# Kernel tuning notes

Hardware: AMD Instinct MI355X
Metric: run time of the kernel (lower is better)

## Reference

```python
import jax, jax.numpy as jnp
import numpy as np

MAX_IT = 10
LAMBDA_ROF = 4.0
SIGMA = 1.0 / (7.0 * 0.01)
TAU = 0.01
THETA = 0.5
M, N = 2048, 2048


def forward_grad(x):
    """x: [1,M,N] -> [2,M,N]; forward differences, zero at last col/row."""
    gh = jnp.pad(x[0, :, 1:] - x[0, :, :-1], ((0, 0), (0, 1)))  # horizontal
    gv = jnp.pad(x[0, 1:, :] - x[0, :-1, :], ((0, 1), (0, 0)))  # vertical
    return jnp.stack([gh, gv], axis=0)


def backward_div(y):
    """y: [2,M,N] -> [1,M,N]; adjoint backward-difference divergence."""
    yh, yv = y[0], y[1]
    d_h = jnp.concatenate([yh[:, :1], yh[:, 1:-1] - yh[:, :-2], -yh[:, -2:-1]], axis=1)
    d_v = jnp.concatenate([yv[:1, :], yv[1:-1, :] - yv[:-2, :], -yv[-2:-1, :]], axis=0)
    return (d_h + d_v)[None]  # [1,M,N]


def prox_linf_ball(p, r):
    # Torch original builds m1/m2 from p.data (no grad flow) -> stop_gradient.
    m1 = jnp.maximum(p - r, 0.0)
    m2 = jnp.maximum(-p - r, 0.0)
    return p - jax.lax.stop_gradient(m1 - m2)  # == clamp(p, -r, r) in value


def setup_inputs() -> dict:
    key = jax.random.key(0)
    k1, k2 = jax.random.split(key)
    img_obs = jax.random.uniform(k1, (1, M, N), dtype=jnp.float32)
    w1 = jnp.array([0.5], dtype=jnp.float32)  # nn.Parameter [1]
    w2 = jnp.array([0.4], dtype=jnp.float32)  # nn.Parameter [1]
    return {"img_obs": img_obs, "w1": w1, "w2": w2}


def reference(img_obs, w1, w2):
    x = img_obs
    x_tilde = img_obs
    y = forward_grad(x)  # [2,M,N]
    # w_term built from y.data in torch -> constant wrt autodiff
    w_term = jax.lax.stop_gradient(jnp.exp(-jnp.abs(y)))
    w = w1[0] + w2[0] * w_term  # [2,M,N]
    for _ in range(MAX_IT):
        # dual weighted update + L-inf prox
        y = y + SIGMA * w * forward_grad(x_tilde)
        y = prox_linf_ball(y, 1.0)
        # primal weighted update (ROF)
        x_old = x
        x = (x + TAU * backward_div(w * y) + LAMBDA_ROF * TAU * img_obs) / (1.0 + LAMBDA_ROF * TAU)
        # primal over-relaxation
        x_tilde = x + THETA * (x - x_old)
    return x_tilde
```

## Files before the change

### kernel.cpp

```cpp
#include <hip/hip_runtime.h>


namespace {
constexpr int M = 2048, N = 2048;
constexpr float SIGMA     = 1.0f / (7.0f * 0.01f);
constexpr float TAUIS     = 0.01f * (7.0f * 0.01f);
constexpr float LT        = 4.0f * 0.01f;
constexpr float INV_DEN   = 1.0f / (1.0f + 4.0f * 0.01f);
constexpr float TAUIS_ID  = TAUIS * INV_DEN;
constexpr float LT_ID     = LT * INV_DEN;
constexpr int TW = 64, TH = 64;
constexpr int PC = 88;
constexpr int PR = 84;
constexpr int UPR = 22;
constexpr int PROC = 83;
constexpr int NU = PROC * UPR;
constexpr int NT = 1024;
constexpr int NPASS = 2;
constexpr int GY = M / TH;
}

typedef _Float16 h4 __attribute__((ext_vector_type(4)));
typedef float    f2 __attribute__((ext_vector_type(2)));
typedef unsigned uint32;

__device__ inline h4 h4splat(float v) {
    _Float16 s = (_Float16)v;
    return (h4){s, s, s, s};
}
__device__ inline int imax(int a, int b) { return a > b ? a : b; }
__device__ inline uint32 abit(uint32 hi, uint32 lo) {
    return __builtin_amdgcn_alignbit(hi, lo, 16);
}
__device__ inline h4 clamp1(h4 v) {
    return __builtin_elementwise_min(
               __builtin_elementwise_max(v, h4splat(-1.f)), h4splat(1.f));
}
__device__ inline uint32 pkrtz(float a, float b) {
    return __builtin_bit_cast(uint32, __builtin_amdgcn_cvt_pkrtz(a, b));
}

__global__ __launch_bounds__(NT, 8) void pd_fused(
    const float* __restrict__ img, float* __restrict__ out,
    const float* __restrict__ w1p, const float* __restrict__ w2p)
{
    __shared__ __align__(16) _Float16 sXT16[PR * PC];
    __shared__ __align__(16) _Float16 sQV[PR * PC];
    __shared__ __align__(16) _Float16 sCI[PR * PC];
    __shared__ __align__(16) _Float16 sSW[2 * PR * PC];
    __shared__ __align__(16) _Float16 sQH3[1840];

    const int tid  = threadIdx.x;
    const int c0 = blockIdx.x * TW, r0 = blockIdx.y * TH;
    const int gr0 = r0 - 10, gc0 = c0 - 12;
    const float w1 = w1p[0], w2 = w2p[0];

    int dth_[NPASS];
    #pragma unroll
    for (int p = 0; p < NPASS; ++p) {
        int u = tid + p * NT;
        int li = u / UPR, lc = (u - li * UPR) * 4;
        int d = imax(imax(9 - li, li - (TH + 9)), imax(8 - lc, lc - 75));
        d = imax(d, 0);
        if (u >= NU) d = 100;
        dth_[p] = d;
    }

    #pragma unroll
    for (int p = 0; p < NPASS; ++p) {
        int su = tid + p * NT;
        if (su < PR * UPR) {
            int li = su / UPR, uj = su - li * UPR;
            int gi = gr0 + li, gj = gc0 + uj * 4;
            float4 v = make_float4(0.f, 0.f, 0.f, 0.f);
            if ((unsigned)gi < (unsigned)M && (unsigned)gj <= (unsigned)(N - 4))
                v = *(const float4*)&img[(size_t)gi * N + gj];
            h4 h; h[0] = (_Float16)v.x; h[1] = (_Float16)v.y;
                  h[2] = (_Float16)v.z; h[3] = (_Float16)v.w;
            *(h4*)&sXT16[su * 4] = h;
        }
    }
    __syncthreads();

    f2 xr2[NPASS][2];
    h4 xt16[NPASS], yh[NPASS], yv[NPASS], qH[NPASS], qvr[NPASS];

    #pragma unroll
    for (int p = 0; p < NPASS; ++p) {
        int u = tid + p * NT;
        if (u < NU) {
            int bF = u * 4;
            int li = u / UPR;
            int gi = gr0 + li, gjb = gc0 + (u - li * UPR) * 4;
            h4 c16 = *(const h4*)&sXT16[bF];
            uint32 rrp = *(const uint32*)&sXT16[bF + 4];
            h4 dn = *(const h4*)&sXT16[bF + PC];
            uint2 xu = __builtin_bit_cast(uint2, c16);
            h4 xsh = __builtin_bit_cast(h4,
                         make_uint2(abit(xu.y, xu.x), abit(rrp, xu.y)));
            bool rok = (unsigned)gi < (unsigned)M;
            bool vok = rok && (gi < M - 1);
            h4 qv, swhv, swvv, civ;
            #pragma unroll
            for (int l = 0; l < 4; ++l) {
                int gj = gjb + l;
                bool cok = (unsigned)gj < (unsigned)N;
                bool hok = rok && cok && (gj < N - 1);
                bool vk  = vok && cok;
                float xf  = (float)c16[l];
                float ghf = hok ? (float)xsh[l] - xf : 0.f;
                float gvf = vk  ? (float)dn[l]  - xf : 0.f;
                float wh = fmaf(w2, __expf(-fabsf(ghf)), w1);
                float wv = fmaf(w2, __expf(-fabsf(gvf)), w1);
                float y0h = fminf(fmaxf(ghf * fmaf(SIGMA, wh, 1.f), -1.f), 1.f);
                float y0v = fminf(fmaxf(gvf * fmaf(SIGMA, wv, 1.f), -1.f), 1.f);
                float sh = hok ? SIGMA * wh : 0.f;
                float sv = vk  ? SIGMA * wv : 0.f;
                yh[p][l]   = (_Float16)y0h;  yv[p][l] = (_Float16)y0v;
                swhv[l]    = (_Float16)sh;   swvv[l]  = (_Float16)sv;
                qH[p][l]   = (_Float16)(sh * y0h);
                qv[l]      = (_Float16)(sv * y0v);
                civ[l]     = (_Float16)(LT_ID * xf);
                xr2[p][l >> 1][l & 1] = xf;
            }
            xt16[p] = c16;
            qvr[p]  = qv;
            *(h4*)&sSW[bF * 2]     = swhv;
            *(h4*)&sSW[bF * 2 + 4] = swvv;
            *(h4*)&sCI[bF]  = civ;
            *(h4*)&sQV[bF]  = qv;
            sQH3[u] = qH[p][3];
        }
    }
    __syncthreads();

    auto dual = [&](int rem) {
        #pragma unroll
        for (int p = 0; p < NPASS; ++p) {
            if (rem >= dth_[p]) {
                int bF = (tid + p * NT) * 4;
                uint32 rrp = *(const uint32*)&sXT16[bF + 4];
                h4 dn  = *(const h4*)&sXT16[bF + PC];
                uint4 swp = *(const uint4*)&sSW[bF * 2];
                h4 swh = __builtin_bit_cast(h4, make_uint2(swp.x, swp.y));
                h4 swv = __builtin_bit_cast(h4, make_uint2(swp.z, swp.w));
                uint2 xu = __builtin_bit_cast(uint2, xt16[p]);
                h4 xsh = __builtin_bit_cast(h4,
                             make_uint2(abit(xu.y, xu.x), abit(rrp, xu.y)));
                h4 ghh = xsh - xt16[p];
                h4 gvh = dn  - xt16[p];
                h4 nh = clamp1(yh[p] + swh * ghh);
                h4 nv = clamp1(yv[p] + swv * gvh);
                yh[p] = nh; yv[p] = nv;
                h4 qh = swh * nh;
                h4 qv = swv * nv;
                qH[p] = qh; qvr[p] = qv;
                *(h4*)&sQV[bF] = qv;
                sQH3[bF >> 2] = qh[3];
            }
        }
    };

    const f2 kID  = {INV_DEN,  INV_DEN};
    const f2 k15  = {1.5f, 1.5f};
    const f2 km05 = {-0.5f, -0.5f};
    const h4 kTS16 = h4splat(TAUIS_ID);
    auto primal = [&](int rem, bool last) {
        #pragma unroll
        for (int p = 0; p < NPASS; ++p) {
            if (rem >= dth_[p]) {
                int u = tid + p * NT, bF = u * 4;
                int bu = (bF >= UPR * 4) ? bF - PC : bF;
                h4 qvu = *(const h4*)&sQV[bu];
                h4 civ = *(const h4*)&sCI[bF];
                uint32 qhl = *(const unsigned short*)&sQH3[imax(u - 1, 0)];
                uint2 qu = __builtin_bit_cast(uint2, qH[p]);
                h4 qsh = __builtin_bit_cast(h4,
                             make_uint2(abit(qu.x, qhl << 16), abit(qu.y, qu.x)));
                h4 dvg = (qH[p] - qsh) + (qvr[p] - qvu);
                h4 s16 = kTS16 * dvg + civ;
                f2 s0 = {(float)s16[0], (float)s16[1]};
                f2 s1 = {(float)s16[2], (float)s16[3]};
                f2 xo0 = xr2[p][0], xo1 = xr2[p][1];
                f2 xn0 = __builtin_elementwise_fma(kID, xo0, s0);
                f2 xn1 = __builtin_elementwise_fma(kID, xo1, s1);
                xr2[p][0] = xn0; xr2[p][1] = xn1;
                f2 xt0 = __builtin_elementwise_fma(k15, xn0, xo0 * km05);
                f2 xt1 = __builtin_elementwise_fma(k15, xn1, xo1 * km05);
                if (!last) {
                    h4 nx = __builtin_bit_cast(h4,
                        make_uint2(pkrtz(xt0[0], xt0[1]),
                                   pkrtz(xt1[0], xt1[1])));
                    xt16[p] = nx;
                    *(h4*)&sXT16[bF] = nx;
                } else {
                    int li = u / UPR, uj = u - li * UPR;
                    int gi = gr0 + li;
                    if (li >= 10 && uj >= 3 && uj <= 18 && gi < M) {
                        *(float4*)&out[(size_t)gi * N + (gc0 + uj * 4)] =
                            make_float4(xt0[0], xt0[1], xt1[0], xt1[1]);
                    }
                }
            }
        }
    };

    primal(9, false);
    __syncthreads();
    #pragma unroll 1
    for (int t = 1; t < 10; ++t) {
        int rem = 9 - t;
        dual(rem);
        __syncthreads();
        primal(rem, t == 9);
        __syncthreads();
    }
}

extern "C" void kernel_launch(void* const* d_in, const int* in_sizes, int n_in,
                              void* d_out, int out_size, void* d_ws, size_t ws_size,
                              hipStream_t stream)
{
    const float* img = (const float*)d_in[0];
    const float* w1  = (const float*)d_in[1];
    const float* w2  = (const float*)d_in[2];
    float* out = (float*)d_out;

    dim3 grid(N / TW, GY);
    pd_fused<<<grid, NT, 0, stream>>>(img, out, w1, w2);
}
```

Baseline: 106.1 us.

## Iterate on deviation from input image in fp16, drop fp32 primal state

The primal state is reformulated as z = x - img. The constant term LT*img cancels, so the per-pixel constant load from shared memory goes away, and the primal update becomes pure packed fp16 arithmetic without fp32 conversions. The initial image gradients are kept in registers and added to the gradient of the deviation in the dual step. The image is added back only when the output is written. This cuts shared loads and conversion instructions, but adds two h4 registers per pass and keeps the whole primal recurrence in fp16, which may cost accuracy. The last iteration is also peeled out of the loop.

```diff
diff --git a/kernel.cpp b/kernel.cpp
--- a/kernel.cpp
+++ b/kernel.cpp
@@ -8,7 +8,6 @@
 constexpr float LT        = 4.0f * 0.01f;
 constexpr float INV_DEN   = 1.0f / (1.0f + 4.0f * 0.01f);
 constexpr float TAUIS_ID  = TAUIS * INV_DEN;
-constexpr float LT_ID     = LT * INV_DEN;
 constexpr int TW = 64, TH = 64;
 constexpr int PC = 88;
 constexpr int PR = 84;
@@ -36,9 +35,6 @@
     return __builtin_elementwise_min(
                __builtin_elementwise_max(v, h4splat(-1.f)), h4splat(1.f));
 }
-__device__ inline uint32 pkrtz(float a, float b) {
-    return __builtin_bit_cast(uint32, __builtin_amdgcn_cvt_pkrtz(a, b));
-}
 
 __global__ __launch_bounds__(NT, 8) void pd_fused(
     const float* __restrict__ img, float* __restrict__ out,
@@ -46,7 +42,7 @@
 {
     __shared__ __align__(16) _Float16 sXT16[PR * PC];
     __shared__ __align__(16) _Float16 sQV[PR * PC];
-    __shared__ __align__(16) _Float16 sCI[PR * PC];
+    __shared__ __align__(16) _Float16 sIM[PR * PC];
     __shared__ __align__(16) _Float16 sSW[2 * PR * PC];
     __shared__ __align__(16) _Float16 sQH3[1840];
 
@@ -82,8 +78,8 @@
     }
     __syncthreads();
 
-    f2 xr2[NPASS][2];
-    h4 xt16[NPASS], yh[NPASS], yv[NPASS], qH[NPASS], qvr[NPASS];
+    h4 zr[NPASS], wt16[NPASS], yh[NPASS], yv[NPASS],
+       qH[NPASS], qvr[NPASS], gih[NPASS], giv[NPASS];
 
     #pragma unroll
     for (int p = 0; p < NPASS; ++p) {
@@ -100,7 +96,7 @@
                          make_uint2(abit(xu.y, xu.x), abit(rrp, xu.y)));
             bool rok = (unsigned)gi < (unsigned)M;
             bool vok = rok && (gi < M - 1);
-            h4 qv, swhv, swvv, civ;
+            h4 qv, swhv, swvv, gh16, gv16;
             #pragma unroll
             for (int l = 0; l < 4; ++l) {
                 int gj = gjb + l;
@@ -120,14 +116,14 @@
                 swhv[l]    = (_Float16)sh;   swvv[l]  = (_Float16)sv;
                 qH[p][l]   = (_Float16)(sh * y0h);
                 qv[l]      = (_Float16)(sv * y0v);
-                civ[l]     = (_Float16)(LT_ID * xf);
-                xr2[p][l >> 1][l & 1] = xf;
+                gh16[l]    = (_Float16)ghf;  gv16[l]  = (_Float16)gvf;
             }
-            xt16[p] = c16;
-            qvr[p]  = qv;
+            gih[p] = gh16; giv[p] = gv16;
+            zr[p]  = h4splat(0.f);
+            qvr[p] = qv;
             *(h4*)&sSW[bF * 2]     = swhv;
             *(h4*)&sSW[bF * 2 + 4] = swvv;
-            *(h4*)&sCI[bF]  = civ;
+            *(h4*)&sIM[bF]  = c16;
             *(h4*)&sQV[bF]  = qv;
             sQH3[u] = qH[p][3];
         }
@@ -144,11 +140,11 @@
                 uint4 swp = *(const uint4*)&sSW[bF * 2];
                 h4 swh = __builtin_bit_cast(h4, make_uint2(swp.x, swp.y));
                 h4 swv = __builtin_bit_cast(h4, make_uint2(swp.z, swp.w));
-                uint2 xu = __builtin_bit_cast(uint2, xt16[p]);
-                h4 xsh = __builtin_bit_cast(h4,
+                uint2 xu = __builtin_bit_cast(uint2, wt16[p]);
+                h4 wsh = __builtin_bit_cast(h4,
                              make_uint2(abit(xu.y, xu.x), abit(rrp, xu.y)));
-                h4 ghh = xsh - xt16[p];
-                h4 gvh = dn  - xt16[p];
+                h4 ghh = (wsh - wt16[p]) + gih[p];
+                h4 gvh = (dn  - wt16[p]) + giv[p];
                 h4 nh = clamp1(yh[p] + swh * ghh);
                 h4 nv = clamp1(yv[p] + swv * gvh);
                 yh[p] = nh; yv[p] = nv;
@@ -161,10 +157,10 @@
         }
     };
 
-    const f2 kID  = {INV_DEN,  INV_DEN};
-    const f2 k15  = {1.5f, 1.5f};
-    const f2 km05 = {-0.5f, -0.5f};
-    const h4 kTS16 = h4splat(TAUIS_ID);
+    const h4 kIDh  = h4splat(INV_DEN);
+    const h4 kTSh  = h4splat(TAUIS_ID);
+    const h4 k15h  = h4splat(1.5f);
+    const h4 km05h = h4splat(-0.5f);
     auto primal = [&](int rem, bool last) {
         #pragma unroll
         for (int p = 0; p < NPASS; ++p) {
@@ -172,33 +168,28 @@
                 int u = tid + p * NT, bF = u * 4;
                 int bu = (bF >= UPR * 4) ? bF - PC : bF;
                 h4 qvu = *(const h4*)&sQV[bu];
-                h4 civ = *(const h4*)&sCI[bF];
                 uint32 qhl = *(const unsigned short*)&sQH3[imax(u - 1, 0)];
                 uint2 qu = __builtin_bit_cast(uint2, qH[p]);
                 h4 qsh = __builtin_bit_cast(h4,
                              make_uint2(abit(qu.x, qhl << 16), abit(qu.y, qu.x)));
                 h4 dvg = (qH[p] - qsh) + (qvr[p] - qvu);
-                h4 s16 = kTS16 * dvg + civ;
-                f2 s0 = {(float)s16[0], (float)s16[1]};
-                f2 s1 = {(float)s16[2], (float)s16[3]};
-                f2 xo0 = xr2[p][0], xo1 = xr2[p][1];
-                f2 xn0 = __builtin_elementwise_fma(kID, xo0, s0);
-                f2 xn1 = __builtin_elementwise_fma(kID, xo1, s1);
-                xr2[p][0] = xn0; xr2[p][1] = xn1;
-                f2 xt0 = __builtin_elementwise_fma(k15, xn0, xo0 * km05);
-                f2 xt1 = __builtin_elementwise_fma(k15, xn1, xo1 * km05);
+                h4 zo = zr[p];
+                h4 zn = kIDh * zo + kTSh * dvg;
+                zr[p] = zn;
+                h4 wt = k15h * zn + km05h * zo;
                 if (!last) {
-                    h4 nx = __builtin_bit_cast(h4,
-                        make_uint2(pkrtz(xt0[0], xt0[1]),
-                                   pkrtz(xt1[0], xt1[1])));
-                    xt16[p] = nx;
-                    *(h4*)&sXT16[bF] = nx;
+                    wt16[p] = wt;
+                    *(h4*)&sXT16[bF] = wt;
                 } else {
                     int li = u / UPR, uj = u - li * UPR;
                     int gi = gr0 + li;
                     if (li >= 10 && uj >= 3 && uj <= 18 && gi < M) {
+                        h4 im = *(const h4*)&sIM[bF];
                         *(float4*)&out[(size_t)gi * N + (gc0 + uj * 4)] =
-                            make_float4(xt0[0], xt0[1], xt1[0], xt1[1]);
+                            make_float4((float)wt[0] + (float)im[0],
+                                        (float)wt[1] + (float)im[1],
+                                        (float)wt[2] + (float)im[2],
+                                        (float)wt[3] + (float)im[3]);
                     }
                 }
             }
@@ -208,13 +199,16 @@
     primal(9, false);
     __syncthreads();
     #pragma unroll 1
-    for (int t = 1; t < 10; ++t) {
+    for (int t = 1; t < 9; ++t) {
         int rem = 9 - t;
         dual(rem);
         __syncthreads();
-        primal(rem, t == 9);
+        primal(rem, false);
         __syncthreads();
     }
+    dual(0);
+    __syncthreads();
+    primal(0, true);
 }
 
 extern "C" void kernel_launch(void* const* d_in, const int* in_sizes, int n_in,
```

Measured after the change: 107.5 us. No clear change (+1.3%).
